# Kernel tuning notes

Hardware: AMD Instinct MI355X
Metric: run time of the kernel (lower is better)

Reference implementation:

```python
import jax, jax.numpy as jnp
import numpy as np

EPS = 1e-7  # K.epsilon()

_LC = np.zeros((3, 3, 3), np.float32)  # Levi-Civita for 1x1->1
_LC[0, 1, 2] = _LC[1, 2, 0] = _LC[2, 0, 1] = 1.0
_LC[0, 2, 1] = _LC[2, 1, 0] = _LC[1, 0, 2] = -1.0


def _ssp(x):
    # shifted softplus: log(0.5*exp(x)+0.5)
    return jnp.log(0.5 * jnp.exp(x) + 0.5)


def _radial(image, w1, b1, w2, b2):
    # Sequential([Dense(32), Dense(feat)]) -- linear Dense layers (no activation)
    return (image @ w1 + b1) @ w2 + b2  # (m, a, b, feat)


def setup_inputs() -> dict:
    key = jax.random.key(0)
    ks = jax.random.split(key, 16)
    M, A, RBF, F, SI, H = 4, 256, 64, 32, 32, 32
    inp = {}
    inp["image"] = jax.random.uniform(ks[0], (M, A, A, RBF), dtype=jnp.float32)
    inp["vectors"] = jax.random.normal(ks[1], (M, A, A, 3), dtype=jnp.float32)
    inp["feat0"] = jax.random.normal(ks[2], (M, A, F, 1), dtype=jnp.float32)
    inp["feat1"] = jax.random.normal(ks[3], (M, A, F, 3), dtype=jnp.float32)
    i = 4
    for rin in (0, 1):
        for fro in (0, 1):
            tag = f"{rin}{fro}"
            inp[f"w1_{tag}"] = jax.random.normal(ks[i], (RBF, H)) / np.sqrt(RBF).astype(np.float32)
            inp[f"b1_{tag}"] = jnp.zeros((H,), jnp.float32)
            i += 1
            inp[f"w2_{tag}"] = jax.random.normal(ks[i], (H, F)) / np.sqrt(np.float32(H))
            inp[f"b2_{tag}"] = jnp.zeros((F,), jnp.float32)
            i += 1
    inp["w_si0"] = jax.random.normal(ks[i], (SI, 2 * F)) / np.sqrt(np.float32(2 * F)); i += 1
    inp["w_si1"] = jax.random.normal(ks[i], (SI, 3 * F)) / np.sqrt(np.float32(3 * F)); i += 1
    inp["b_act0"] = jnp.zeros((SI,), jnp.float32)
    inp["b_act1"] = jnp.zeros((SI,), jnp.float32)
    return inp


def reference(image, vectors, feat0, feat1,
              w1_00, b1_00, w2_00, b2_00,
              w1_01, b1_01, w2_01, b2_01,
              w1_10, b1_10, w2_10, b2_10,
              w1_11, b1_11, w2_11, b2_11,
              w_si0, w_si1, b_act0, b_act1):
    # mask where |r_ab| < eps (self-pairs / padding)
    mask = (jnp.sqrt(jnp.sum(vectors * vectors, axis=-1)) < EPS)[..., None]  # (m,a,b,1)

    def filt0(w1, b1, w2, b2):
        return _radial(image, w1, b1, w2, b2)  # (m,a,b,F), implicit rep index of size 1

    def filt1(w1, b1, w2, b2):
        r = jnp.where(mask, 0.0, _radial(image, w1, b1, w2, b2))  # masked radial
        return vectors[:, :, :, None, :] * r[..., None]  # (m,a,b,F,3)

    f0_in0 = filt0(w1_00, b1_00, w2_00, b2_00)
    f1_in0 = filt1(w1_01, b1_01, w2_01, b2_01)
    f0_in1 = filt0(w1_10, b1_10, w2_10, b2_10)
    f1_in1 = filt1(w1_11, b1_11, w2_11, b2_11)

    # point convolution (sum over neighbor atoms b)
    out_0x0_0 = jnp.einsum('mabf,mbfj->mafj', f0_in0, feat0)   # (m,a,F,1)
    out_0x1_1 = jnp.einsum('mabfi,mbfj->mafi', f1_in0, feat0)  # (m,a,F,3)
    out_1x0_1 = jnp.einsum('mabf,mbfj->mafj', f0_in1, feat1)   # (m,a,F,3)
    cg0 = jnp.eye(3, dtype=image.dtype)[None]                  # (1,3,3): 1x1->0
    out_1x1_0 = jnp.einsum('ijk,mabfj,mbfk->mafi', cg0, f1_in1, feat1)  # (m,a,F,1)
    lc = jnp.asarray(_LC, image.dtype)                         # 1x1->1
    out_1x1_1 = jnp.einsum('ijk,mabfj,mbfk->mafi', lc, f1_in1, feat1)   # (m,a,F,3)

    # concat along channel dim per output RO
    cat0 = jnp.concatenate([out_0x0_0, out_1x1_0], axis=2)  # (m,a,2F,1)
    cat1 = jnp.concatenate([out_0x1_1, out_1x0_1, out_1x1_1], axis=2)  # (m,a,3F,3)

    # self-interaction: einsum('mafi,gf->maig') then transpose -> (m,a,g,i)
    si0 = jnp.einsum('mafi,gf->magi', cat0, w_si0)  # (m,a,SI,1)
    si1 = jnp.einsum('mafi,gf->magi', cat1, w_si1)  # (m,a,SI,3)

    # equivariant activation
    o0 = _ssp(si0 + b_act0[None, None, :, None])
    n1 = jnp.sqrt(jnp.maximum(jnp.sum(si1 * si1, axis=-1), EPS))  # norm_with_epsilon
    a1 = _ssp(n1 + b_act1)
    o1 = si1 * (a1 / n1)[..., None]
    return (o0, o1)
```

## Files before the change

kernel.cpp:

```cpp
#include <hip/hip_runtime.h>
#include <math.h>

#define M_ 4
#define A_ 256
#define RBF_ 64
#define F_ 32
#define H_ 32
#define SI_ 32
#define TF_ 128
#define SASTRIDE 158

typedef __attribute__((ext_vector_type(8))) short bf16x8;
typedef __attribute__((ext_vector_type(4))) float f32x4;
typedef __attribute__((ext_vector_type(3))) float f32x3;

__device__ __forceinline__ unsigned short f2bf(float f) {
  union { float f; unsigned u; } v; v.f = f;
  unsigned r = v.u + 0x7FFFu + ((v.u >> 16) & 1u);
  return (unsigned short)(r >> 16);
}

__device__ __forceinline__ unsigned pack2bf(float lo, float hi) {
  union { float f; unsigned u; } a, b; a.f = lo; b.f = hi;
  return __builtin_amdgcn_perm(b.u + 0x8000u, a.u + 0x8000u, 0x07060302u);
}

__device__ __forceinline__ float sspf(float x) {
  return fmaxf(x, 0.f) + log1pf(expf(-fabsf(x))) - 0.6931471805599453f;
}

__global__ __launch_bounds__(256) void combine_weights(
    const float* __restrict__ w1_00, const float* __restrict__ b1_00,
    const float* __restrict__ w2_00, const float* __restrict__ b2_00,
    const float* __restrict__ w1_01, const float* __restrict__ b1_01,
    const float* __restrict__ w2_01, const float* __restrict__ b2_01,
    const float* __restrict__ w1_10, const float* __restrict__ b1_10,
    const float* __restrict__ w2_10, const float* __restrict__ b2_10,
    const float* __restrict__ w1_11, const float* __restrict__ b1_11,
    const float* __restrict__ w2_11, const float* __restrict__ b2_11,
    unsigned short* __restrict__ wsT, float* __restrict__ bcw)
{
  const float* w1s[4] = {w1_00, w1_01, w1_10, w1_11};
  const float* b1s[4] = {b1_00, b1_01, b1_10, b1_11};
  const float* w2s[4] = {w2_00, w2_01, w2_10, w2_11};
  const float* b2s[4] = {b2_00, b2_01, b2_10, b2_11};
  int tid = blockIdx.x * 256 + threadIdx.x;
  int k   = tid >> 7;
  int tf  = tid & 127;
  int tag = tf >> 5, f = tf & 31;
  const float* w1 = w1s[tag];
  const float* w2 = w2s[tag];
  float s = 0.f;
  for (int h = 0; h < H_; ++h) s += w1[k * H_ + h] * w2[h * F_ + f];
  wsT[tf * 64 + k] = f2bf(s);
  if (tid < TF_) {
    const float* b1 = b1s[tag];
    const float* b2 = b2s[tag];
    float sb = b2[f];
    for (int h = 0; h < H_; ++h) sb += b1[h] * w2[h * F_ + f];
    bcw[tf] = sb;
  }
}

__global__ __launch_bounds__(512, 4) void conv_partial(
    const float* __restrict__ image, const float* __restrict__ vectors,
    const float* __restrict__ feat0, const float* __restrict__ feat1,
    const unsigned short* __restrict__ wsT, const float* __restrict__ bcw,
    float* __restrict__ part)
{
  __shared__ __align__(16) unsigned short sA[128 * SASTRIDE];
  __shared__ float sV[128 * 3];

  const int t    = threadIdx.x;
  const int bid  = blockIdx.x;
  const int ma   = bid >> 1;
  const int half = bid & 1;
  const int m    = ma >> 8;
  const int l    = t & 63;
  const int n    = l & 15;
  const int quad = l >> 4;
  const int wu    = __builtin_amdgcn_readfirstlane(t >> 6);
  const int which = wu & 1;
  const int tag   = wu >> 1;
  const int ct    = tag * 2 + which;
  const int f     = which * 16 + n;

  const unsigned short* wr = wsT + (ct * 16 + n) * 64 + quad * 8;
  const bf16x8 w0 = *(const bf16x8*)(wr);
  const bf16x8 w1 = *(const bf16x8*)(wr + 32);
  const float  bc = bcw[ct * 16 + n];

  const float* imgH = image + ((size_t)ma * A_ + half * 128) * RBF_;
  #pragma unroll
  for (int i = 0; i < 2; ++i) {
    int g = t + 512 * i;
    int r = g >> 3, c8 = g & 7;
    const float* src = imgH + r * RBF_ + c8 * 8;
    float4 v0 = *(const float4*)(src);
    float4 v1 = *(const float4*)(src + 4);
    uint4 pk;
    pk.x = pack2bf(v0.x, v0.y);
    pk.y = pack2bf(v0.z, v0.w);
    pk.z = pack2bf(v1.x, v1.y);
    pk.w = pack2bf(v1.z, v1.w);
    *(uint4*)&sA[r * SASTRIDE + c8 * 8] = pk;
  }
  if (t < 384) sV[t] = vectors[((size_t)ma * A_ + half * 128) * 3 + t];

  const float* p0 = feat0 + (size_t)(m * A_) * F_ + f;
  const float* p1 = feat1 + ((size_t)(m * A_) * F_ + f) * 3;

  float gxA[4], gyA[4], gzA[4];
  float gxB[4], gyB[4], gzB[4];
  float pA = 0.f, pB0 = 0.f, pB1 = 0.f, pB2 = 0.f;

#define PF(GX, GY, GZ, BT) { \
    const int b0 = half * 128 + (BT) * 16 + quad * 4; \
    if (tag <= 1) { \
      _Pragma("unroll") \
      for (int r = 0; r < 4; ++r) GX[r] = p0[(b0 + r) * F_]; \
    } else { \
      _Pragma("unroll") \
      for (int r = 0; r < 4; ++r) { \
        f32x3 v = *(const f32x3*)&p1[(size_t)(b0 + r) * (F_ * 3)]; \
        GX[r] = v[0]; GY[r] = v[1]; GZ[r] = v[2]; \
      } \
    } }

#define BODY(BT, GX, GY, GZ) { \
    const int brow = (BT) * 16; \
    const int lb   = brow + quad * 4; \
    const bf16x8 a0 = *(const bf16x8*)&sA[(brow + n) * SASTRIDE + quad * 8]; \
    const bf16x8 a1 = *(const bf16x8*)&sA[(brow + n) * SASTRIDE + 32 + quad * 8]; \
    f32x4 acc = {bc, bc, bc, bc}; \
    acc = __builtin_amdgcn_mfma_f32_16x16x32_bf16(a0, w0, acc, 0, 0, 0); \
    acc = __builtin_amdgcn_mfma_f32_16x16x32_bf16(a1, w1, acc, 0, 0, 0); \
    if (tag == 0) {             \
      _Pragma("unroll") \
      for (int r = 0; r < 4; ++r) pA += acc[r] * GX[r]; \
    } else if (tag == 1) {      \
      _Pragma("unroll") \
      for (int r = 0; r < 4; ++r) { \
        const float s  = acc[r] * GX[r]; \
        pB0 += sV[(lb + r) * 3 + 0] * s; \
        pB1 += sV[(lb + r) * 3 + 1] * s; \
        pB2 += sV[(lb + r) * 3 + 2] * s; \
      } \
    } else if (tag == 2) {      \
      _Pragma("unroll") \
      for (int r = 0; r < 4; ++r) { \
        const float Rr = acc[r]; \
        pB0 += Rr * GX[r]; pB1 += Rr * GY[r]; pB2 += Rr * GZ[r]; \
      } \
    } else {                    \
      _Pragma("unroll") \
      for (int r = 0; r < 4; ++r) { \
        const float Rr = acc[r]; \
        const float ax = GX[r], ay = GY[r], az = GZ[r]; \
        const float vx = sV[(lb + r) * 3 + 0]; \
        const float vy = sV[(lb + r) * 3 + 1]; \
        const float vz = sV[(lb + r) * 3 + 2]; \
        pA  += Rr * (vx * ax + vy * ay + vz * az); \
        pB0 += Rr * (vy * az - vz * ay); \
        pB1 += Rr * (vz * ax - vx * az); \
        pB2 += Rr * (vx * ay - vy * ax); \
      } \
    } }

  PF(gxA, gyA, gzA, 0)
  PF(gxB, gyB, gzB, 4)
  __syncthreads();

  #pragma unroll 1
  for (int it = 0; it < 4; ++it) {
    BODY(it, gxA, gyA, gzA)
    if (it < 3) PF(gxA, gyA, gzA, it + 1)
    BODY(4 + it, gxB, gyB, gzB)
    if (it < 3) PF(gxB, gyB, gzB, 4 + it + 1)
  }

#define QRED(x) { x += __shfl_xor(x, 16); x += __shfl_xor(x, 32); }
  QRED(pA) QRED(pB0) QRED(pB1) QRED(pB2)
  if (quad == 0) {
    float* dst = part + ((size_t)ma * 2 + half) * 352;
    if (tag == 0) {
      dst[f] = pA;
    } else if (tag == 1) {
      f32x3 v = {pB0, pB1, pB2};
      *(f32x3*)&dst[64 + f * 3] = v;
    } else if (tag == 2) {
      f32x3 v = {pB0, pB1, pB2};
      *(f32x3*)&dst[160 + f * 3] = v;
    } else {
      dst[32 + f] = pA;
      f32x3 v = {pB0, pB1, pB2};
      *(f32x3*)&dst[256 + f * 3] = v;
    }
  }
}

__global__ __launch_bounds__(64) void si_epilogue(
    const float* __restrict__ part,
    const float* __restrict__ w_si0, const float* __restrict__ w_si1,
    const float* __restrict__ b_act0, const float* __restrict__ b_act1,
    float* __restrict__ out)
{
  __shared__ float cat[352];
  const int ma = blockIdx.x;
  const int t  = threadIdx.x;
  const float* pA = part + (size_t)ma * 704;
  const float* pB = pA + 352;
  for (int s = t; s < 352; s += 64) cat[s] = pA[s] + pB[s];
  __syncthreads();

  const int outBase = ma * SI_;
  if (t < 32) {
    const float* wr = w_si0 + t * 64;
    float s = 0.f;
    #pragma unroll 8
    for (int ff = 0; ff < 64; ++ff) s += cat[ff] * wr[ff];
    s += b_act0[t];
    out[outBase + t] = sspf(s);
  } else {
    int g = t - 32;
    const float* wr = w_si1 + g * 96;
    float s0 = 0.f, s1 = 0.f, s2 = 0.f;
    #pragma unroll 8
    for (int ff = 0; ff < 96; ++ff) {
      float wv = wr[ff];
      s0 += cat[64 + ff * 3 + 0] * wv;
      s1 += cat[64 + ff * 3 + 1] * wv;
      s2 += cat[64 + ff * 3 + 2] * wv;
    }
    float n2 = s0 * s0 + s1 * s1 + s2 * s2;
    float n1 = sqrtf(fmaxf(n2, 1e-7f));
    float a1 = sspf(n1 + b_act1[g]);
    float sc = a1 / n1;
    int ob = M_ * A_ * SI_ + (outBase + g) * 3;
    out[ob + 0] = s0 * sc;
    out[ob + 1] = s1 * sc;
    out[ob + 2] = s2 * sc;
  }
}

extern "C" void kernel_launch(void* const* d_in, const int* in_sizes, int n_in,
                              void* d_out, int out_size, void* d_ws, size_t ws_size,
                              hipStream_t stream) {
  const float* image   = (const float*)d_in[0];
  const float* vectors = (const float*)d_in[1];
  const float* feat0   = (const float*)d_in[2];
  const float* feat1   = (const float*)d_in[3];
  const float* w_si0   = (const float*)d_in[20];
  const float* w_si1   = (const float*)d_in[21];
  const float* b_act0  = (const float*)d_in[22];
  const float* b_act1  = (const float*)d_in[23];
  unsigned short* wsT = (unsigned short*)d_ws;
  float* bcw  = (float*)((char*)d_ws + 16384);
  float* part = (float*)((char*)d_ws + 32768);
  float* out  = (float*)d_out;

  combine_weights<<<32, 256, 0, stream>>>(
      (const float*)d_in[4],  (const float*)d_in[5],
      (const float*)d_in[6],  (const float*)d_in[7],
      (const float*)d_in[8],  (const float*)d_in[9],
      (const float*)d_in[10], (const float*)d_in[11],
      (const float*)d_in[12], (const float*)d_in[13],
      (const float*)d_in[14], (const float*)d_in[15],
      (const float*)d_in[16], (const float*)d_in[17],
      (const float*)d_in[18], (const float*)d_in[19],
      wsT, bcw);

  conv_partial<<<2 * M_ * A_, 512, 0, stream>>>(
      image, vectors, feat0, feat1, wsT, bcw, part);

  si_epilogue<<<M_ * A_, 64, 0, stream>>>(
      part, w_si0, w_si1, b_act0, b_act1, out);
}
```

Measured before the change: 170.8 us.

## Shrink LDS row stride, rotate wave roles per block, restructure prefetch loop

Reduces the LDS row stride for the bf16 image tile from 158 to 72 elements, which cuts shared memory per block and may let more blocks fit per CU. Wave-to-role assignment is rotated by block index so different tags' global loads and work spread across blocks. The prefetch/compute loop now walks the 128 rows in order with pointer increments and a two-slot buffer instead of two interleaved halves, and the cross-product math uses explicit FMAs. The new stride may change LDS bank conflict patterns on the bf16x8 reads.

```diff
diff --git a/kernel.cpp b/kernel.cpp
--- a/kernel.cpp
+++ b/kernel.cpp
@@ -8,7 +8,6 @@
 #define H_ 32
 #define SI_ 32
 #define TF_ 128
-#define SASTRIDE 158
 
 typedef __attribute__((ext_vector_type(8))) short bf16x8;
 typedef __attribute__((ext_vector_type(4))) float f32x4;
@@ -68,7 +67,7 @@
     const unsigned short* __restrict__ wsT, const float* __restrict__ bcw,
     float* __restrict__ part)
 {
-  __shared__ __align__(16) unsigned short sA[128 * SASTRIDE];
+  __shared__ __align__(16) unsigned short sA[128 * 72];
   __shared__ float sV[128 * 3];
 
   const int t    = threadIdx.x;
@@ -80,8 +79,9 @@
   const int n    = l & 15;
   const int quad = l >> 4;
   const int wu    = __builtin_amdgcn_readfirstlane(t >> 6);
-  const int which = wu & 1;
-  const int tag   = wu >> 1;
+  const int role  = (wu + ((bid & 3) << 1)) & 7;
+  const int which = role & 1;
+  const int tag   = role >> 1;
   const int ct    = tag * 2 + which;
   const int f     = which * 16 + n;
 
@@ -103,35 +103,35 @@
     pk.y = pack2bf(v0.z, v0.w);
     pk.z = pack2bf(v1.x, v1.y);
     pk.w = pack2bf(v1.z, v1.w);
-    *(uint4*)&sA[r * SASTRIDE + c8 * 8] = pk;
+    *(uint4*)&sA[r * 72 + c8 * 8] = pk;
   }
   if (t < 384) sV[t] = vectors[((size_t)ma * A_ + half * 128) * 3 + t];
 
-  const float* p0 = feat0 + (size_t)(m * A_) * F_ + f;
-  const float* p1 = feat1 + ((size_t)(m * A_) * F_ + f) * 3;
-
-  float gxA[4], gyA[4], gzA[4];
-  float gxB[4], gyB[4], gzB[4];
+  const int b0q = half * 128 + quad * 4;
+  const float* p0c = feat0 + (size_t)(m * A_ + b0q) * F_ + f;
+  const float* p1c = feat1 + ((size_t)(m * A_ + b0q) * F_ + f) * 3;
+  const float* svc = &sV[quad * 4 * 3];
+  const unsigned short* aBc = &sA[n * 72 + quad * 8];
+
+  float gx[2][4], gy[2][4], gz[2][4];
   float pA = 0.f, pB0 = 0.f, pB1 = 0.f, pB2 = 0.f;
 
-#define PF(GX, GY, GZ, BT) { \
-    const int b0 = half * 128 + (BT) * 16 + quad * 4; \
+#define PF(BUF) { \
     if (tag <= 1) { \
       _Pragma("unroll") \
-      for (int r = 0; r < 4; ++r) GX[r] = p0[(b0 + r) * F_]; \
+      for (int r = 0; r < 4; ++r) gx[BUF][r] = p0c[r * F_]; \
     } else { \
       _Pragma("unroll") \
       for (int r = 0; r < 4; ++r) { \
-        f32x3 v = *(const f32x3*)&p1[(size_t)(b0 + r) * (F_ * 3)]; \
-        GX[r] = v[0]; GY[r] = v[1]; GZ[r] = v[2]; \
-      } \
-    } }
-
-#define BODY(BT, GX, GY, GZ) { \
-    const int brow = (BT) * 16; \
-    const int lb   = brow + quad * 4; \
-    const bf16x8 a0 = *(const bf16x8*)&sA[(brow + n) * SASTRIDE + quad * 8]; \
-    const bf16x8 a1 = *(const bf16x8*)&sA[(brow + n) * SASTRIDE + 32 + quad * 8]; \
+        f32x3 v = *(const f32x3*)(p1c + r * (F_ * 3)); \
+        gx[BUF][r] = v[0]; gy[BUF][r] = v[1]; gz[BUF][r] = v[2]; \
+      } \
+    } \
+    p0c += 16 * F_; p1c += 16 * F_ * 3; }
+
+#define BODY(AOFF, SOFF, GX, GY, GZ) { \
+    const bf16x8 a0 = *(const bf16x8*)(aBc + (AOFF)); \
+    const bf16x8 a1 = *(const bf16x8*)(aBc + (AOFF) + 32); \
     f32x4 acc = {bc, bc, bc, bc}; \
     acc = __builtin_amdgcn_mfma_f32_16x16x32_bf16(a0, w0, acc, 0, 0, 0); \
     acc = __builtin_amdgcn_mfma_f32_16x16x32_bf16(a1, w1, acc, 0, 0, 0); \
@@ -141,10 +141,10 @@
     } else if (tag == 1) {      \
       _Pragma("unroll") \
       for (int r = 0; r < 4; ++r) { \
-        const float s  = acc[r] * GX[r]; \
-        pB0 += sV[(lb + r) * 3 + 0] * s; \
-        pB1 += sV[(lb + r) * 3 + 1] * s; \
-        pB2 += sV[(lb + r) * 3 + 2] * s; \
+        const float s = acc[r] * GX[r]; \
+        pB0 += svc[(SOFF) + r * 3 + 0] * s; \
+        pB1 += svc[(SOFF) + r * 3 + 1] * s; \
+        pB2 += svc[(SOFF) + r * 3 + 2] * s; \
       } \
     } else if (tag == 2) {      \
       _Pragma("unroll") \
@@ -157,26 +157,28 @@
       for (int r = 0; r < 4; ++r) { \
         const float Rr = acc[r]; \
         const float ax = GX[r], ay = GY[r], az = GZ[r]; \
-        const float vx = sV[(lb + r) * 3 + 0]; \
-        const float vy = sV[(lb + r) * 3 + 1]; \
-        const float vz = sV[(lb + r) * 3 + 2]; \
-        pA  += Rr * (vx * ax + vy * ay + vz * az); \
-        pB0 += Rr * (vy * az - vz * ay); \
-        pB1 += Rr * (vz * ax - vx * az); \
-        pB2 += Rr * (vx * ay - vy * ax); \
+        const float vx = svc[(SOFF) + r * 3 + 0]; \
+        const float vy = svc[(SOFF) + r * 3 + 1]; \
+        const float vz = svc[(SOFF) + r * 3 + 2]; \
+        float d = vx * ax; d = fmaf(vy, ay, d); d = fmaf(vz, az, d); \
+        pA = fmaf(Rr, d, pA); \
+        float c0 = vy * az; c0 = fmaf(-vz, ay, c0); pB0 = fmaf(Rr, c0, pB0); \
+        float c1 = vz * ax; c1 = fmaf(-vx, az, c1); pB1 = fmaf(Rr, c1, pB1); \
+        float c2 = vx * ay; c2 = fmaf(-vy, ax, c2); pB2 = fmaf(Rr, c2, pB2); \
       } \
     } }
 
-  PF(gxA, gyA, gzA, 0)
-  PF(gxB, gyB, gzB, 4)
+  PF(0)
   __syncthreads();
 
   #pragma unroll 1
   for (int it = 0; it < 4; ++it) {
-    BODY(it, gxA, gyA, gzA)
-    if (it < 3) PF(gxA, gyA, gzA, it + 1)
-    BODY(4 + it, gxB, gyB, gzB)
-    if (it < 3) PF(gxB, gyB, gzB, 4 + it + 1)
+    PF(1)
+    BODY(0, 0, gx[0], gy[0], gz[0])
+    if (it < 3) PF(0)
+    BODY(1152, 48, gx[1], gy[1], gz[1])
+    aBc += 2 * 1152;
+    svc += 2 * 48;
   }
 
 #define QRED(x) { x += __shfl_xor(x, 16); x += __shfl_xor(x, 32); }
```

Result: faster. 161.3 us (-5.5%).
